# Kernel tuning notes

Hardware: AMD Instinct MI355X
Metric: run time of the kernel (lower is better)

Reference implementation:

```python
import jax, jax.numpy as jnp
import numpy as np

N = 1048576   # total points
C = 64        # in_planes
B = 16        # number of batch segments
EPS = 1e-5    # BatchNorm eps


def setup_inputs() -> dict:
    key = jax.random.key(0)
    ks = jax.random.split(key, 10)
    x = jax.random.normal(ks[0], (N, C), dtype=jnp.float32)
    # cumulative offsets: equal-size segments, o[-1] == N
    o = (jnp.arange(1, B + 1, dtype=jnp.int32) * (N // B))
    # linear2: Linear(C, C) + ReLU
    W2 = jax.random.normal(ks[1], (C, C), dtype=jnp.float32) / np.sqrt(C)
    b2 = jax.random.normal(ks[2], (C,), dtype=jnp.float32) * 0.01
    # linear1: Linear(2C, C) + BatchNorm1d(C) + ReLU (BN in eval mode)
    W1 = jax.random.normal(ks[3], (2 * C, C), dtype=jnp.float32) / np.sqrt(2 * C)
    b1 = jax.random.normal(ks[4], (C,), dtype=jnp.float32) * 0.01
    gamma = jnp.ones((C,), dtype=jnp.float32)
    beta = jnp.zeros((C,), dtype=jnp.float32)
    run_mean = jax.random.normal(ks[5], (C,), dtype=jnp.float32) * 0.1
    run_var = jax.random.uniform(ks[6], (C,), dtype=jnp.float32, minval=0.5, maxval=1.5)
    return {"x": x, "o": o, "W2": W2, "b2": b2, "W1": W1, "b1": b1,
            "gamma": gamma, "beta": beta, "run_mean": run_mean, "run_var": run_var}


def reference(x, o, W2, b2, W1, b1, gamma, beta, run_mean, run_var):
    n = x.shape[0]
    # segment id of each point from cumulative offsets
    seg = jnp.searchsorted(o, jnp.arange(n, dtype=o.dtype), side="right")  # [N]
    counts = jnp.diff(o, prepend=jnp.zeros((1,), dtype=o.dtype))           # [B]
    # per-segment sum-pool -> mean
    sums = jax.ops.segment_sum(x, seg, num_segments=B)                     # [B, C]
    mean = sums / counts[:, None].astype(x.dtype)                          # [B, C]
    # linear2 + ReLU on the tiny [B, C] pooled features
    h = jax.nn.relu(mean @ W2 + b2)                                        # [B, C]
    # broadcast back to points and concat -> [N, 2C]
    cat = jnp.concatenate([x, h[seg]], axis=1)
    # linear1 + BatchNorm1d (eval mode) + ReLU
    z = cat @ W1 + b1                                                      # [N, C]
    z = (z - run_mean) * jax.lax.rsqrt(run_var + EPS) * gamma + beta
    return jax.nn.relu(z)
```

## Files before the change

kernel.cpp:

```cpp
#include <hip/hip_runtime.h>


#define MAXB 16

typedef _Float16 half8 __attribute__((ext_vector_type(8)));
typedef float float4v __attribute__((ext_vector_type(4)));

__global__ __launch_bounds__(256) void pool_kernel(
    const float* __restrict__ x, const int* __restrict__ o,
    float* __restrict__ gsums, int nB, int ptsPerBlock) {
  __shared__ int so_s[MAXB];
  __shared__ float red[16 * 64];
  __shared__ float ssum2[MAXB * 64];
  const int tid = threadIdx.x;
  if (tid < nB) so_s[tid] = o[tid];
  __syncthreads();

  const int c4 = (tid & 15) * 4;
  const int r  = tid >> 4;
  const int p0 = blockIdx.x * ptsPerBlock;
  const int iters = ptsPerBlock >> 4;

  int sFirst = 0;
  while (p0 >= so_s[sFirst]) sFirst++;
  int sLast = sFirst;
  while (p0 + ptsPerBlock - 1 >= so_s[sLast]) sLast++;

  if (sFirst == sLast) {
    float a0 = 0.f, a1 = 0.f, a2 = 0.f, a3 = 0.f;
    const float* xp = x + (size_t)(p0 + r) * 64 + c4;
#pragma unroll 4
    for (int i = 0; i < iters; ++i) {
      float4 v = *(const float4*)(xp + (size_t)i * 1024);
      a0 += v.x; a1 += v.y; a2 += v.z; a3 += v.w;
    }
    float4 t = {a0, a1, a2, a3};
    *(float4*)&red[r * 64 + c4] = t;
    __syncthreads();
    if (tid < 64) {
      float s = 0.f;
#pragma unroll
      for (int rr = 0; rr < 16; ++rr) s += red[rr * 64 + tid];
      atomicAdd(&gsums[sFirst * 64 + tid], s);
    }
  } else {
    for (int i = tid; i < nB * 64; i += 256) ssum2[i] = 0.f;
    __syncthreads();
    for (int i = 0; i < iters; ++i) {
      int p = p0 + i * 16 + r;
      int s = 0;
      while (p >= so_s[s]) s++;
      float4 v = *(const float4*)(x + (size_t)p * 64 + c4);
      atomicAdd(&ssum2[s * 64 + c4 + 0], v.x);
      atomicAdd(&ssum2[s * 64 + c4 + 1], v.y);
      atomicAdd(&ssum2[s * 64 + c4 + 2], v.z);
      atomicAdd(&ssum2[s * 64 + c4 + 3], v.w);
    }
    __syncthreads();
    for (int i = tid; i < nB * 64; i += 256) {
      float v = ssum2[i];
      if (v != 0.f) atomicAdd(&gsums[i], v);
    }
  }
}

__global__ __launch_bounds__(256) void mid_kernel(
    const float* __restrict__ gsums, const int* __restrict__ o,
    const float* __restrict__ W2, const float* __restrict__ b2,
    const float* __restrict__ W1, const float* __restrict__ b1,
    const float* __restrict__ gamma, const float* __restrict__ beta,
    const float* __restrict__ rmean, const float* __restrict__ rvar,
    float* __restrict__ biasp, _Float16* __restrict__ WpT, int nB) {
  __shared__ float smean[MAXB * 64];
  __shared__ float sh[MAXB * 64];
  const int tid = threadIdx.x;
  const int j = tid & 63;
  const int bq = tid >> 6;

  for (int i = tid; i < nB * 64; i += 256) {
    int b = i >> 6;
    int cnt = o[b] - (b ? o[b - 1] : 0);
    smean[i] = gsums[i] / (float)cnt;
  }
  __syncthreads();

  for (int b = bq; b < nB; b += 4) {
    float p0 = 0.f, p1 = 0.f, p2 = 0.f, p3 = 0.f;
#pragma unroll
    for (int c = 0; c < 64; c += 4) {
      p0 = fmaf(smean[b * 64 + c + 0], W2[(c + 0) * 64 + j], p0);
      p1 = fmaf(smean[b * 64 + c + 1], W2[(c + 1) * 64 + j], p1);
      p2 = fmaf(smean[b * 64 + c + 2], W2[(c + 2) * 64 + j], p2);
      p3 = fmaf(smean[b * 64 + c + 3], W2[(c + 3) * 64 + j], p3);
    }
    sh[b * 64 + j] = fmaxf(((p0 + p1) + (p2 + p3)) + b2[j], 0.f);
  }
  __syncthreads();

  const float a = gamma[j] * rsqrtf(rvar[j] + 1e-5f);
  const float d = beta[j] - rmean[j] * a;
  for (int b = bq; b < nB; b += 4) {
    float p0 = 0.f, p1 = 0.f, p2 = 0.f, p3 = 0.f;
#pragma unroll
    for (int c = 0; c < 64; c += 4) {
      p0 = fmaf(sh[b * 64 + c + 0], W1[(64 + c + 0) * 64 + j], p0);
      p1 = fmaf(sh[b * 64 + c + 1], W1[(64 + c + 1) * 64 + j], p1);
      p2 = fmaf(sh[b * 64 + c + 2], W1[(64 + c + 2) * 64 + j], p2);
      p3 = fmaf(sh[b * 64 + c + 3], W1[(64 + c + 3) * 64 + j], p3);
    }
    biasp[b * 64 + j] = (((p0 + p1) + (p2 + p3)) + b1[j]) * a + d;
  }
  for (int k = bq * 16; k < bq * 16 + 16; ++k)
    WpT[j * 64 + k] = (_Float16)(W1[k * 64 + j] * a);
}

__global__ __launch_bounds__(256) void main_kernel(
    const float* __restrict__ x, const int* __restrict__ o,
    const _Float16* __restrict__ WpT, const float* __restrict__ biasp,
    float* __restrict__ out, int nB) {
  const int lane = threadIdx.x & 63;
  const int m = lane & 15;
  const int quad = lane >> 4;
  const int rows0 = (blockIdx.x * 4 + (threadIdx.x >> 6)) * 128;

  half8 bfrag[4][2];
#pragma unroll
  for (int t = 0; t < 4; ++t)
#pragma unroll
    for (int h = 0; h < 2; ++h)
      bfrag[t][h] = *(const half8*)(WpT + (t * 16 + m) * 64 + h * 32 + quad * 8);

  const int ov = (m < nB) ? o[m] : 0x7fffffff;

  float4 f0, f1, f2, f3;
  {
    const float* p = x + (size_t)(rows0 + m) * 64 + quad * 8;
    f0 = *(const float4*)(p + 0);
    f1 = *(const float4*)(p + 4);
    f2 = *(const float4*)(p + 32);
    f3 = *(const float4*)(p + 36);
  }

  for (int i = 0; i < 8; ++i) {
    const int row0 = rows0 + i * 16;
    half8 a0, a1;
    a0[0] = (_Float16)f0.x; a0[1] = (_Float16)f0.y;
    a0[2] = (_Float16)f0.z; a0[3] = (_Float16)f0.w;
    a0[4] = (_Float16)f1.x; a0[5] = (_Float16)f1.y;
    a0[6] = (_Float16)f1.z; a0[7] = (_Float16)f1.w;
    a1[0] = (_Float16)f2.x; a1[1] = (_Float16)f2.y;
    a1[2] = (_Float16)f2.z; a1[3] = (_Float16)f2.w;
    a1[4] = (_Float16)f3.x; a1[5] = (_Float16)f3.y;
    a1[6] = (_Float16)f3.z; a1[7] = (_Float16)f3.w;

    if (i < 7) {
      const float* p = x + (size_t)(row0 + 16 + m) * 64 + quad * 8;
      f0 = *(const float4*)(p + 0);
      f1 = *(const float4*)(p + 4);
      f2 = *(const float4*)(p + 32);
      f3 = *(const float4*)(p + 36);
    }

    const int s0 = (int)__popcll(__ballot(row0 >= ov) & 0xFFFFull);
    const int s1 = (int)__popcll(__ballot(row0 + 15 >= ov) & 0xFFFFull);

    if (s0 == s1) {
      const float* bp = biasp + s0 * 64 + m;
#pragma unroll
      for (int t = 0; t < 4; ++t) {
        float4v c = {0.f, 0.f, 0.f, 0.f};
        c = __builtin_amdgcn_mfma_f32_16x16x32_f16(a0, bfrag[t][0], c, 0, 0, 0);
        c = __builtin_amdgcn_mfma_f32_16x16x32_f16(a1, bfrag[t][1], c, 0, 0, 0);
        const float bv = bp[t * 16];
        float* op = out + (size_t)(row0 + quad * 4) * 64 + t * 16 + m;
#pragma unroll
        for (int rg = 0; rg < 4; ++rg)
          op[(size_t)rg * 64] = fmaxf(c[rg] + bv, 0.f);
      }
    } else {
#pragma unroll
      for (int t = 0; t < 4; ++t) {
        float4v c = {0.f, 0.f, 0.f, 0.f};
        c = __builtin_amdgcn_mfma_f32_16x16x32_f16(a0, bfrag[t][0], c, 0, 0, 0);
        c = __builtin_amdgcn_mfma_f32_16x16x32_f16(a1, bfrag[t][1], c, 0, 0, 0);
#pragma unroll
        for (int rg = 0; rg < 4; ++rg) {
          const int row = row0 + quad * 4 + rg;
          int s = 0;
          for (int q2 = 0; q2 < nB; ++q2) s += (row >= o[q2]) ? 1 : 0;
          const float bv = biasp[s * 64 + t * 16 + m];
          out[(size_t)row * 64 + t * 16 + m] = fmaxf(c[rg] + bv, 0.f);
        }
      }
    }
  }
}

extern "C" void kernel_launch(void* const* d_in, const int* in_sizes, int n_in,
                              void* d_out, int out_size, void* d_ws, size_t ws_size,
                              hipStream_t stream) {
  const float* x     = (const float*)d_in[0];
  const int*   o     = (const int*)d_in[1];
  const float* W2    = (const float*)d_in[2];
  const float* b2    = (const float*)d_in[3];
  const float* W1    = (const float*)d_in[4];
  const float* b1    = (const float*)d_in[5];
  const float* gamma = (const float*)d_in[6];
  const float* beta  = (const float*)d_in[7];
  const float* rmean = (const float*)d_in[8];
  const float* rvar  = (const float*)d_in[9];
  float* out = (float*)d_out;

  const int npts = in_sizes[0] / 64;
  const int nB   = in_sizes[1];

  float*    gsums = (float*)d_ws;
  float*    biasp = gsums + MAXB * 64;
  _Float16* WpT   = (_Float16*)(biasp + MAXB * 64);

  hipMemsetAsync(gsums, 0, MAXB * 64 * sizeof(float), stream);

  const int blocks1 = 2048;
  pool_kernel<<<blocks1, 256, 0, stream>>>(x, o, gsums, nB, npts / blocks1);
  mid_kernel<<<1, 256, 0, stream>>>(gsums, o, W2, b2, W1, b1, gamma, beta,
                                    rmean, rvar, biasp, WpT, nB);
  main_kernel<<<npts / 512, 256, 0, stream>>>(x, o, WpT, biasp, out, nB);
}
```

Before: 522.0 us.

## Fuse pooling with matmul, store fp16 pre-bias result, add bias in separate pass

Computes the x·W1 projection (BN-scaled) inside the pooling pass so x is read only once, writing an fp16 intermediate z. A separate kernel then adds the per-segment bias and ReLU, reading z and writing the fp32 output with nontemporal stores. Total memory traffic stays similar because the fp16 intermediate is written and reread, and it adds rounding of the pre-bias result to fp16.

```diff
diff --git a/kernel.cpp b/kernel.cpp
--- a/kernel.cpp
+++ b/kernel.cpp
@@ -6,55 +6,126 @@
 typedef _Float16 half8 __attribute__((ext_vector_type(8)));
 typedef float float4v __attribute__((ext_vector_type(4)));
 
-__global__ __launch_bounds__(256) void pool_kernel(
+__global__ __launch_bounds__(256) void fuse_kernel(
     const float* __restrict__ x, const int* __restrict__ o,
-    float* __restrict__ gsums, int nB, int ptsPerBlock) {
+    const float* __restrict__ W1, const float* __restrict__ gamma,
+    const float* __restrict__ rvar,
+    float* __restrict__ gsums, _Float16* __restrict__ z,
+    int nB, int ptsPerBlock) {
   __shared__ int so_s[MAXB];
-  __shared__ float red[16 * 64];
+  __shared__ float red[4 * 64];
   __shared__ float ssum2[MAXB * 64];
   const int tid = threadIdx.x;
   if (tid < nB) so_s[tid] = o[tid];
   __syncthreads();
 
-  const int c4 = (tid & 15) * 4;
-  const int r  = tid >> 4;
+  const int lane = tid & 63;
+  const int m = lane & 15;
+  const int quad = lane >> 4;
+  const int w = tid >> 6;
   const int p0 = blockIdx.x * ptsPerBlock;
-  const int iters = ptsPerBlock >> 4;
+  const int rows0 = p0 + w * 128;
+
+  half8 bfrag[4][2];
+#pragma unroll
+  for (int t = 0; t < 4; ++t) {
+    const int n = t * 16 + m;
+    const float a = gamma[n] * rsqrtf(rvar[n] + 1e-5f);
+#pragma unroll
+    for (int h = 0; h < 2; ++h)
+#pragma unroll
+      for (int jj = 0; jj < 8; ++jj)
+        bfrag[t][h][jj] = (_Float16)(W1[(h * 32 + quad * 8 + jj) * 64 + n] * a);
+  }
 
   int sFirst = 0;
   while (p0 >= so_s[sFirst]) sFirst++;
   int sLast = sFirst;
   while (p0 + ptsPerBlock - 1 >= so_s[sLast]) sLast++;
-
-  if (sFirst == sLast) {
-    float a0 = 0.f, a1 = 0.f, a2 = 0.f, a3 = 0.f;
-    const float* xp = x + (size_t)(p0 + r) * 64 + c4;
-#pragma unroll 4
-    for (int i = 0; i < iters; ++i) {
-      float4 v = *(const float4*)(xp + (size_t)i * 1024);
-      a0 += v.x; a1 += v.y; a2 += v.z; a3 += v.w;
-    }
-    float4 t = {a0, a1, a2, a3};
-    *(float4*)&red[r * 64 + c4] = t;
+  const bool uniform = (sFirst == sLast);
+
+  float4v s0 = {0.f, 0.f, 0.f, 0.f}, s1 = s0, s2 = s0, s3 = s0;
+
+  float4v f0, f1, f2, f3;
+  {
+    const float* p = x + (size_t)(rows0 + m) * 64 + quad * 8;
+    f0 = __builtin_nontemporal_load((const float4v*)(p + 0));
+    f1 = __builtin_nontemporal_load((const float4v*)(p + 4));
+    f2 = __builtin_nontemporal_load((const float4v*)(p + 32));
+    f3 = __builtin_nontemporal_load((const float4v*)(p + 36));
+  }
+
+  for (int i = 0; i < 8; ++i) {
+    const int row0 = rows0 + i * 16;
+    s0 += f0; s1 += f1; s2 += f2; s3 += f3;
+
+    half8 a0, a1;
+    a0[0] = (_Float16)f0[0]; a0[1] = (_Float16)f0[1];
+    a0[2] = (_Float16)f0[2]; a0[3] = (_Float16)f0[3];
+    a0[4] = (_Float16)f1[0]; a0[5] = (_Float16)f1[1];
+    a0[6] = (_Float16)f1[2]; a0[7] = (_Float16)f1[3];
+    a1[0] = (_Float16)f2[0]; a1[1] = (_Float16)f2[1];
+    a1[2] = (_Float16)f2[2]; a1[3] = (_Float16)f2[3];
+    a1[4] = (_Float16)f3[0]; a1[5] = (_Float16)f3[1];
+    a1[6] = (_Float16)f3[2]; a1[7] = (_Float16)f3[3];
+
+    if (i < 7) {
+      const float* p = x + (size_t)(row0 + 16 + m) * 64 + quad * 8;
+      f0 = __builtin_nontemporal_load((const float4v*)(p + 0));
+      f1 = __builtin_nontemporal_load((const float4v*)(p + 4));
+      f2 = __builtin_nontemporal_load((const float4v*)(p + 32));
+      f3 = __builtin_nontemporal_load((const float4v*)(p + 36));
+    }
+
+#pragma unroll
+    for (int t = 0; t < 4; ++t) {
+      float4v c = {0.f, 0.f, 0.f, 0.f};
+      c = __builtin_amdgcn_mfma_f32_16x16x32_f16(a0, bfrag[t][0], c, 0, 0, 0);
+      c = __builtin_amdgcn_mfma_f32_16x16x32_f16(a1, bfrag[t][1], c, 0, 0, 0);
+      _Float16* zp = z + (size_t)(row0 + quad * 4) * 64 + t * 16 + m;
+#pragma unroll
+      for (int rg = 0; rg < 4; ++rg)
+        zp[(size_t)rg * 64] = (_Float16)c[rg];
+    }
+  }
+
+  if (uniform) {
+#pragma unroll
+    for (int mask = 1; mask < 16; mask <<= 1) {
+#pragma unroll
+      for (int k = 0; k < 4; ++k) {
+        s0[k] += __shfl_xor(s0[k], mask);
+        s1[k] += __shfl_xor(s1[k], mask);
+        s2[k] += __shfl_xor(s2[k], mask);
+        s3[k] += __shfl_xor(s3[k], mask);
+      }
+    }
+    if (m == 0) {
+      *(float4v*)&red[w * 64 + quad * 8 + 0] = s0;
+      *(float4v*)&red[w * 64 + quad * 8 + 4] = s1;
+      *(float4v*)&red[w * 64 + 32 + quad * 8 + 0] = s2;
+      *(float4v*)&red[w * 64 + 32 + quad * 8 + 4] = s3;
+    }
     __syncthreads();
     if (tid < 64) {
-      float s = 0.f;
-#pragma unroll
-      for (int rr = 0; rr < 16; ++rr) s += red[rr * 64 + tid];
+      float s = red[tid] + red[64 + tid] + red[128 + tid] + red[192 + tid];
       atomicAdd(&gsums[sFirst * 64 + tid], s);
     }
   } else {
+    const int c4 = (tid & 15) * 4;
+    const int r  = tid >> 4;
+    const int iters = ptsPerBlock >> 4;
     for (int i = tid; i < nB * 64; i += 256) ssum2[i] = 0.f;
     __syncthreads();
     for (int i = 0; i < iters; ++i) {
       int p = p0 + i * 16 + r;
       int s = 0;
       while (p >= so_s[s]) s++;
-      float4 v = *(const float4*)(x + (size_t)p * 64 + c4);
-      atomicAdd(&ssum2[s * 64 + c4 + 0], v.x);
-      atomicAdd(&ssum2[s * 64 + c4 + 1], v.y);
-      atomicAdd(&ssum2[s * 64 + c4 + 2], v.z);
-      atomicAdd(&ssum2[s * 64 + c4 + 3], v.w);
+      float4v v = *(const float4v*)(x + (size_t)p * 64 + c4);
+      atomicAdd(&ssum2[s * 64 + c4 + 0], v[0]);
+      atomicAdd(&ssum2[s * 64 + c4 + 1], v[1]);
+      atomicAdd(&ssum2[s * 64 + c4 + 2], v[2]);
+      atomicAdd(&ssum2[s * 64 + c4 + 3], v[3]);
     }
     __syncthreads();
     for (int i = tid; i < nB * 64; i += 256) {
@@ -70,7 +141,7 @@
     const float* __restrict__ W1, const float* __restrict__ b1,
     const float* __restrict__ gamma, const float* __restrict__ beta,
     const float* __restrict__ rmean, const float* __restrict__ rvar,
-    float* __restrict__ biasp, _Float16* __restrict__ WpT, int nB) {
+    float* __restrict__ biasp, int nB) {
   __shared__ float smean[MAXB * 64];
   __shared__ float sh[MAXB * 64];
   const int tid = threadIdx.x;
@@ -110,88 +181,67 @@
     }
     biasp[b * 64 + j] = (((p0 + p1) + (p2 + p3)) + b1[j]) * a + d;
   }
-  for (int k = bq * 16; k < bq * 16 + 16; ++k)
-    WpT[j * 64 + k] = (_Float16)(W1[k * 64 + j] * a);
-}
-
-__global__ __launch_bounds__(256) void main_kernel(
-    const float* __restrict__ x, const int* __restrict__ o,
-    const _Float16* __restrict__ WpT, const float* __restrict__ biasp,
-    float* __restrict__ out, int nB) {
-  const int lane = threadIdx.x & 63;
-  const int m = lane & 15;
-  const int quad = lane >> 4;
-  const int rows0 = (blockIdx.x * 4 + (threadIdx.x >> 6)) * 128;
-
-  half8 bfrag[4][2];
-#pragma unroll
-  for (int t = 0; t < 4; ++t)
-#pragma unroll
-    for (int h = 0; h < 2; ++h)
-      bfrag[t][h] = *(const half8*)(WpT + (t * 16 + m) * 64 + h * 32 + quad * 8);
-
-  const int ov = (m < nB) ? o[m] : 0x7fffffff;
-
-  float4 f0, f1, f2, f3;
-  {
-    const float* p = x + (size_t)(rows0 + m) * 64 + quad * 8;
-    f0 = *(const float4*)(p + 0);
-    f1 = *(const float4*)(p + 4);
-    f2 = *(const float4*)(p + 32);
-    f3 = *(const float4*)(p + 36);
-  }
-
-  for (int i = 0; i < 8; ++i) {
-    const int row0 = rows0 + i * 16;
-    half8 a0, a1;
-    a0[0] = (_Float16)f0.x; a0[1] = (_Float16)f0.y;
-    a0[2] = (_Float16)f0.z; a0[3] = (_Float16)f0.w;
-    a0[4] = (_Float16)f1.x; a0[5] = (_Float16)f1.y;
-    a0[6] = (_Float16)f1.z; a0[7] = (_Float16)f1.w;
-    a1[0] = (_Float16)f2.x; a1[1] = (_Float16)f2.y;
-    a1[2] = (_Float16)f2.z; a1[3] = (_Float16)f2.w;
-    a1[4] = (_Float16)f3.x; a1[5] = (_Float16)f3.y;
-    a1[6] = (_Float16)f3.z; a1[7] = (_Float16)f3.w;
-
-    if (i < 7) {
-      const float* p = x + (size_t)(row0 + 16 + m) * 64 + quad * 8;
-      f0 = *(const float4*)(p + 0);
-      f1 = *(const float4*)(p + 4);
-      f2 = *(const float4*)(p + 32);
-      f3 = *(const float4*)(p + 36);
-    }
-
-    const int s0 = (int)__popcll(__ballot(row0 >= ov) & 0xFFFFull);
-    const int s1 = (int)__popcll(__ballot(row0 + 15 >= ov) & 0xFFFFull);
-
-    if (s0 == s1) {
-      const float* bp = biasp + s0 * 64 + m;
-#pragma unroll
-      for (int t = 0; t < 4; ++t) {
-        float4v c = {0.f, 0.f, 0.f, 0.f};
-        c = __builtin_amdgcn_mfma_f32_16x16x32_f16(a0, bfrag[t][0], c, 0, 0, 0);
-        c = __builtin_amdgcn_mfma_f32_16x16x32_f16(a1, bfrag[t][1], c, 0, 0, 0);
-        const float bv = bp[t * 16];
-        float* op = out + (size_t)(row0 + quad * 4) * 64 + t * 16 + m;
-#pragma unroll
-        for (int rg = 0; rg < 4; ++rg)
-          op[(size_t)rg * 64] = fmaxf(c[rg] + bv, 0.f);
-      }
-    } else {
-#pragma unroll
-      for (int t = 0; t < 4; ++t) {
-        float4v c = {0.f, 0.f, 0.f, 0.f};
-        c = __builtin_amdgcn_mfma_f32_16x16x32_f16(a0, bfrag[t][0], c, 0, 0, 0);
-        c = __builtin_amdgcn_mfma_f32_16x16x32_f16(a1, bfrag[t][1], c, 0, 0, 0);
-#pragma unroll
-        for (int rg = 0; rg < 4; ++rg) {
-          const int row = row0 + quad * 4 + rg;
-          int s = 0;
-          for (int q2 = 0; q2 < nB; ++q2) s += (row >= o[q2]) ? 1 : 0;
-          const float bv = biasp[s * 64 + t * 16 + m];
-          out[(size_t)row * 64 + t * 16 + m] = fmaxf(c[rg] + bv, 0.f);
-        }
-      }
+}
+
+__global__ __launch_bounds__(256) void bias_kernel(
+    const _Float16* __restrict__ z, const int* __restrict__ o,
+    const float* __restrict__ biasp, float* __restrict__ out,
+    int nB, int rowsPerBlock) {
+  __shared__ int so_s[MAXB];
+  const int tid = threadIdx.x;
+  if (tid < nB) so_s[tid] = o[tid];
+  __syncthreads();
+
+  const int c8 = (tid & 7) * 8;
+  const int rr = tid >> 3;
+  const int p0 = blockIdx.x * rowsPerBlock;
+  const int iters = rowsPerBlock >> 5;
+
+  int sFirst = 0;
+  while (p0 >= so_s[sFirst]) sFirst++;
+  int sLast = sFirst;
+  while (p0 + rowsPerBlock - 1 >= so_s[sLast]) sLast++;
+
+  if (sFirst == sLast) {
+    const float4v b0 = *(const float4v*)(biasp + sFirst * 64 + c8);
+    const float4v b1 = *(const float4v*)(biasp + sFirst * 64 + c8 + 4);
+#pragma unroll 4
+    for (int i = 0; i < iters; ++i) {
+      const int row = p0 + i * 32 + rr;
+      half8 v = *(const half8*)(z + (size_t)row * 64 + c8);
+      float4v r0, r1;
+      r0[0] = fmaxf((float)v[0] + b0[0], 0.f);
+      r0[1] = fmaxf((float)v[1] + b0[1], 0.f);
+      r0[2] = fmaxf((float)v[2] + b0[2], 0.f);
+      r0[3] = fmaxf((float)v[3] + b0[3], 0.f);
+      r1[0] = fmaxf((float)v[4] + b1[0], 0.f);
+      r1[1] = fmaxf((float)v[5] + b1[1], 0.f);
+      r1[2] = fmaxf((float)v[6] + b1[2], 0.f);
+      r1[3] = fmaxf((float)v[7] + b1[3], 0.f);
+      float* op = out + (size_t)row * 64 + c8;
+      __builtin_nontemporal_store(r0, (float4v*)(op + 0));
+      __builtin_nontemporal_store(r1, (float4v*)(op + 4));
+    }
+  } else {
+    for (int i = 0; i < iters; ++i) {
+      const int row = p0 + i * 32 + rr;
+      int s = 0;
+      for (int q = 0; q < nB; ++q) s += (row >= so_s[q]) ? 1 : 0;
+      const float4v b0 = *(const float4v*)(biasp + s * 64 + c8);
+      const float4v b1 = *(const float4v*)(biasp + s * 64 + c8 + 4);
+      half8 v = *(const half8*)(z + (size_t)row * 64 + c8);
+      float4v r0, r1;
+      r0[0] = fmaxf((float)v[0] + b0[0], 0.f);
+      r0[1] = fmaxf((float)v[1] + b0[1], 0.f);
+      r0[2] = fmaxf((float)v[2] + b0[2], 0.f);
+      r0[3] = fmaxf((float)v[3] + b0[3], 0.f);
+      r1[0] = fmaxf((float)v[4] + b1[0], 0.f);
+      r1[1] = fmaxf((float)v[5] + b1[1], 0.f);
+      r1[2] = fmaxf((float)v[6] + b1[2], 0.f);
+      r1[3] = fmaxf((float)v[7] + b1[3], 0.f);
+      float* op = out + (size_t)row * 64 + c8;
+      __builtin_nontemporal_store(r0, (float4v*)(op + 0));
+      __builtin_nontemporal_store(r1, (float4v*)(op + 4));
     }
   }
 }
@@ -216,13 +266,14 @@
 
   float*    gsums = (float*)d_ws;
   float*    biasp = gsums + MAXB * 64;
-  _Float16* WpT   = (_Float16*)(biasp + MAXB * 64);
+  _Float16* z     = (_Float16*)((char*)d_ws + 8192);
 
   hipMemsetAsync(gsums, 0, MAXB * 64 * sizeof(float), stream);
 
-  const int blocks1 = 2048;
-  pool_kernel<<<blocks1, 256, 0, stream>>>(x, o, gsums, nB, npts / blocks1);
+  const int blocks = 2048;
+  fuse_kernel<<<blocks, 256, 0, stream>>>(x, o, W1, gamma, rvar, gsums, z,
+                                          nB, npts / blocks);
   mid_kernel<<<1, 256, 0, stream>>>(gsums, o, W2, b2, W1, b1, gamma, beta,
-                                    rmean, rvar, biasp, WpT, nB);
-  main_kernel<<<npts / 512, 256, 0, stream>>>(x, o, WpT, biasp, out, nB);
-}
+                                    rmean, rvar, biasp, nB);
+  bias_kernel<<<blocks, 256, 0, stream>>>(z, o, biasp, out, nB, npts / blocks);
+}
```

Measured after the change: 558.3 us. 7.0% more time.
